# Kernel optimization log

Measured on AMD Instinct MI355X. Metric: run time of the kernel, lower is better.

The kernel has to match this reference:

```python
import jax, jax.numpy as jnp
import numpy as np

B, N, D = 16, 1024, 768
H = 12
HD = D // H
HID = 4 * D
EPS = 1e-6


def _layernorm(x, g, b):
    mu = jnp.mean(x, axis=-1, keepdims=True)
    var = jnp.mean(jnp.square(x - mu), axis=-1, keepdims=True)
    return (x - mu) * jax.lax.rsqrt(var + EPS) * g + b


def setup_inputs() -> dict:
    key = jax.random.key(0)
    ks = jax.random.split(key, 8)
    s_d = 1.0 / np.sqrt(D)
    s_h = 1.0 / np.sqrt(HID)
    return {
        "x": jax.random.normal(ks[0], (B, N, D), dtype=jnp.float32),
        "qkv_w": jax.random.uniform(ks[1], (3 * D, D), jnp.float32, -s_d, s_d),
        "proj_w": jax.random.uniform(ks[2], (D, D), jnp.float32, -s_d, s_d),
        "proj_b": jax.random.uniform(ks[3], (D,), jnp.float32, -s_d, s_d),
        "fc1_w": jax.random.uniform(ks[4], (HID, D), jnp.float32, -s_d, s_d),
        "fc1_b": jax.random.uniform(ks[5], (HID,), jnp.float32, -s_d, s_d),
        "fc2_w": jax.random.uniform(ks[6], (D, HID), jnp.float32, -s_h, s_h),
        "fc2_b": jax.random.uniform(ks[7], (D,), jnp.float32, -s_h, s_h),
        "norm1_g": jnp.ones((D,), jnp.float32),
        "norm1_b": jnp.zeros((D,), jnp.float32),
        "norm2_g": jnp.ones((D,), jnp.float32),
        "norm2_b": jnp.zeros((D,), jnp.float32),
    }


def _attention(x, qkv_w, proj_w, proj_b):
    b, n, _ = x.shape
    qkv = x @ qkv_w.T                                  # [b,n,3D] (no bias: qkv_bias=False)
    qkv = qkv.reshape(b, n, 3, H, HD)
    q, k, v = (jnp.transpose(qkv[:, :, i], (0, 2, 1, 3)) for i in range(3))  # [b,h,n,hd]
    scale = HD ** (-0.5)
    dots = jnp.einsum("bhid,bhjd->bhij", q, k) * scale
    attn = jax.nn.softmax(dots, axis=-1)
    out = jnp.einsum("bhij,bhjd->bhid", attn, v)
    out = jnp.transpose(out, (0, 2, 1, 3)).reshape(b, n, H * HD)
    return out @ proj_w.T + proj_b


def _mlp(x, fc1_w, fc1_b, fc2_w, fc2_b):
    h = jax.nn.gelu(x @ fc1_w.T + fc1_b, approximate=False)
    return h @ fc2_w.T + fc2_b


def reference(x, qkv_w, proj_w, proj_b, fc1_w, fc1_b, fc2_w, fc2_b,
              norm1_g, norm1_b, norm2_g, norm2_b):
    x = x + _attention(_layernorm(x, norm1_g, norm1_b), qkv_w, proj_w, proj_b)
    x = x + _mlp(_layernorm(x, norm2_g, norm2_b), fc1_w, fc1_b, fc2_w, fc2_b)
    return x
```

## Files before the change

### kernel.cpp

```cpp
#include <hip/hip_runtime.h>
#include <hip/hip_bf16.h>
#include <math.h>

using bf16 = __hip_bfloat16;
typedef __attribute__((ext_vector_type(8))) short short8;
typedef __attribute__((ext_vector_type(4))) short shortx4;
typedef __attribute__((ext_vector_type(4))) float floatx4;

#define BB 16
#define NN 1024
#define DD 768
#define HH 12
#define HD 64
#define HID 3072

#define QSCALE 0.1803368801f

__device__ __forceinline__ floatx4 mfma_bf16(short8 a, short8 b, floatx4 c) {
  return __builtin_amdgcn_mfma_f32_16x16x32_bf16(a, b, c, 0, 0, 0);
}

__device__ __forceinline__ short bf16_bits(float f) {
  union { bf16 h; short s; } u;
  u.h = __float2bfloat16(f);
  return u.s;
}

__device__ __forceinline__ void async_copy16(const void* g, void* l) {
  __builtin_amdgcn_global_load_lds(
      (const __attribute__((address_space(1))) unsigned int*)g,
      (__attribute__((address_space(3))) unsigned int*)l,
      16, 0, 0);
}

__device__ __forceinline__ float gelu_f(float x) {
  const float z = x * fmaf(0.10294324f, x * x, 2.3022082f);
  const float e = exp2f(z);
  return x - x * __builtin_amdgcn_rcpf(e + 1.0f);
}

__global__ __launch_bounds__(256)
void cvt_kernel(const float* __restrict__ in, bf16* __restrict__ out, int n4)
{
  const int i = blockIdx.x * 256 + threadIdx.x;
  if (i >= n4) return;
  const float4 v = ((const float4*)in)[i];
  shortx4 o;
  o.x = bf16_bits(v.x); o.y = bf16_bits(v.y);
  o.z = bf16_bits(v.z); o.w = bf16_bits(v.w);
  ((shortx4*)out)[i] = o;
}

__global__ __launch_bounds__(256)
void ln_kernel(const float* __restrict__ x, const float* __restrict__ g,
               const float* __restrict__ b, bf16* __restrict__ y)
{
  const int row = blockIdx.x;
  const int t = threadIdx.x;
  const float* xr = x + (size_t)row * DD;
  float v[3];
  float s = 0.f, s2 = 0.f;
#pragma unroll
  for (int i = 0; i < 3; ++i) {
    float f = xr[t + i * 256];
    v[i] = f;
    s += f;
    s2 += f * f;
  }
#pragma unroll
  for (int off = 1; off < 64; off <<= 1) {
    s  += __shfl_xor(s, off);
    s2 += __shfl_xor(s2, off);
  }
  __shared__ float red[2][4];
  const int wave = t >> 6, lane = t & 63;
  if (lane == 0) { red[0][wave] = s; red[1][wave] = s2; }
  __syncthreads();
  s  = red[0][0] + red[0][1] + red[0][2] + red[0][3];
  s2 = red[1][0] + red[1][1] + red[1][2] + red[1][3];
  const float mu = s * (1.f / DD);
  const float var = s2 * (1.f / DD) - mu * mu;
  const float inv = rsqrtf(var + 1e-6f);
  bf16* yr = y + (size_t)row * DD;
#pragma unroll
  for (int i = 0; i < 3; ++i) {
    int c = t + i * 256;
    yr[c] = __float2bfloat16((v[i] - mu) * inv * g[c] + b[c]);
  }
}

template <int EPI>
__global__ __launch_bounds__(256, 4)
void gemm_kernel(const bf16* __restrict__ A, const bf16* __restrict__ W,
                 const float* __restrict__ bias, const float* __restrict__ res,
                 void* __restrict__ Cv, int N, int K)
{
  __shared__ __align__(16) short smem[16896];
  short* sA = smem;
  short* sB = smem + 8192;

  const int tid  = threadIdx.x;
  const int lane = tid & 63;
  const int wave = tid >> 6;
  const int wm = wave & 1, wn = wave >> 1;
  const int row16 = lane & 15, quad = lane >> 4;

  const int lin = blockIdx.y * gridDim.x + blockIdx.x;
  const int per = gridDim.x * 8;
  const int pan = lin / per, rem = lin % per;
  const int bm = (pan * 8 + (rem & 7)) * 128;
  const int bn = (rem >> 3) * 128;

  const int lrow = lane >> 3;
  const int lkc  = (lane & 7) ^ lrow;

  const bf16* Ag = A + (size_t)(bm + wave * 32 + lrow) * K + lkc * 8;
  const bf16* Bg = W + (size_t)(bn + wave * 32 + lrow) * K + lkc * 8;
  short* sAw = sA + wave * 2048;
  short* sBw = sB + wave * 2048;

  floatx4 acc[4][4] = {};

  for (int kt = 0; kt < K; kt += 64) {
#pragma unroll
    for (int g = 0; g < 4; ++g) {
      async_copy16(Ag + (size_t)g * 8 * K + kt, sAw + g * 512);
      async_copy16(Bg + (size_t)g * 8 * K + kt, sBw + g * 512);
    }
    __syncthreads();
#pragma unroll
    for (int c = 0; c < 2; ++c) {
      short8 af[4], bfr[4];
      const int kc = c * 4 + quad;
#pragma unroll
      for (int mt = 0; mt < 4; ++mt) {
        const int row = wm * 64 + mt * 16 + row16;
        af[mt] = *(const short8*)&sA[(row >> 3) * 512 + ((row & 7) * 8 + (kc ^ (row & 7))) * 8];
      }
#pragma unroll
      for (int nt = 0; nt < 4; ++nt) {
        const int row = wn * 64 + nt * 16 + row16;
        bfr[nt] = *(const short8*)&sB[(row >> 3) * 512 + ((row & 7) * 8 + (kc ^ (row & 7))) * 8];
      }
#pragma unroll
      for (int mt = 0; mt < 4; ++mt)
#pragma unroll
        for (int nt = 0; nt < 4; ++nt)
          acc[mt][nt] = mfma_bf16(bfr[nt], af[mt], acc[mt][nt]);
    }
    __syncthreads();
  }

  if (EPI == 1) {
#pragma unroll
    for (int mt = 0; mt < 4; ++mt) {
      const int row = bm + wm * 64 + mt * 16 + row16;
#pragma unroll
      for (int nt = 0; nt < 4; ++nt) {
        const int col = bn + wn * 64 + nt * 16 + quad * 4;
        const floatx4 bv = *(const floatx4*)&bias[col];
        const floatx4 rv = *(const floatx4*)&res[(size_t)row * N + col];
        floatx4 o;
#pragma unroll
        for (int r = 0; r < 4; ++r) o[r] = acc[mt][nt][r] + bv[r] + rv[r];
        *(floatx4*)&((float*)Cv)[(size_t)row * N + col] = o;
      }
    }
  } else {
    short* sC = smem;
#pragma unroll
    for (int mt = 0; mt < 4; ++mt) {
      const int lr = wm * 64 + mt * 16 + row16;
#pragma unroll
      for (int nt = 0; nt < 4; ++nt) {
        const int lc = wn * 64 + nt * 16 + quad * 4;
        floatx4 bv = {};
        if (EPI == 2) bv = *(const floatx4*)&bias[bn + lc];
        shortx4 pk;
#pragma unroll
        for (int r = 0; r < 4; ++r) {
          float v = acc[mt][nt][r] + bv[r];
          if (EPI == 2) v = gelu_f(v);
          if (EPI == 0 && bn + lc < DD) v *= QSCALE;
          pk[r] = bf16_bits(v);
        }
        *(shortx4*)&sC[lr * 132 + lc] = pk;
      }
    }
    __syncthreads();
#pragma unroll
    for (int it = 0; it < 8; ++it) {
      const int row = (tid >> 4) + it * 16;
      const int col = (tid & 15) * 8;
      short8 v = *(const short8*)&sC[row * 132 + col];
      *(short8*)&((bf16*)Cv)[(size_t)(bm + row) * N + bn + col] = v;
    }
  }
}

__global__ __launch_bounds__(256)
void vtrans_kernel(const bf16* __restrict__ qkv, bf16* __restrict__ vt)
{
  const int bh = blockIdx.y;
  const int b = bh / HH, h = bh % HH;
  const int n0 = blockIdx.x * 64;
  __shared__ __align__(16) short tile[64 * 72];
  const int tid = threadIdx.x;

  const int r = tid >> 2, c16 = (tid & 3) * 16;
  const bf16* src = qkv + (size_t)(b * NN + n0 + r) * 2304 + 2 * DD + h * 64 + c16;
  *(short8*)&tile[r * 72 + c16]     = *(const short8*)(src);
  *(short8*)&tile[r * 72 + c16 + 8] = *(const short8*)(src + 8);
  __syncthreads();

#pragma unroll
  for (int it = 0; it < 2; ++it) {
    const int d  = (tid >> 3) + it * 32;
    const int jg = (tid & 7) * 8;
    short8 o;
#pragma unroll
    for (int t = 0; t < 8; ++t) ((short*)&o)[t] = tile[(jg + t) * 72 + d];
    *(short8*)&vt[((size_t)bh * 64 + d) * NN + n0 + jg] = o;
  }
}

__global__ __launch_bounds__(256, 2)
void attn_kernel(const bf16* __restrict__ qkv, const bf16* __restrict__ vt,
                 bf16* __restrict__ out)
{
  const int nbh = gridDim.y;
  const int gx  = gridDim.x;
  int bh, qi;
  if ((nbh & 7) == 0) {
    const int lin = blockIdx.y * gx + blockIdx.x;
    const int xcd = lin & 7;
    const int idx = lin >> 3;
    const int per = nbh >> 3;
    bh = xcd * per + idx / gx;
    qi = idx % gx;
  } else {
    bh = blockIdx.y; qi = blockIdx.x;
  }
  const int b = bh / HH, h = bh % HH;
  const int q0 = qi * 256;
  const int tid = threadIdx.x;
  const int lane = tid & 63;
  const int wave = tid >> 6;
  const int row16 = lane & 15, quad = lane >> 4;

  __shared__ __align__(16) short sK[4096];
  __shared__ __align__(16) short sVt[4096];
  __shared__ __align__(16) short sP[4][4][1024];

  const bf16* base  = qkv + (size_t)b * NN * 2304 + h * 64;
  const bf16* vbase = vt + (size_t)bh * 64 * NN;

  short8 qf[4][2];
#pragma unroll
  for (int qg = 0; qg < 4; ++qg) {
    const bf16* qrow = base + (size_t)(q0 + wave * 64 + qg * 16 + row16) * 2304;
    qf[qg][0] = *(const short8*)(qrow + quad * 8);
    qf[qg][1] = *(const short8*)(qrow + 32 + quad * 8);
  }

  floatx4 o_acc[4][4] = {};
  floatx4 l_acc[4] = {};
  const short8 ones = { (short)0x3F80, (short)0x3F80, (short)0x3F80, (short)0x3F80,
                        (short)0x3F80, (short)0x3F80, (short)0x3F80, (short)0x3F80 };

  const bf16* ksrc = base + DD + (size_t)(wave * 16 + row16) * 2304 + quad * 8;
  const bf16* vsrc = vbase + (size_t)(wave * 16 + row16) * NN + quad * 8;
  short* kdst = sK + wave * 1024 + lane * 8;
  short* vdst = sVt + wave * 1024 + lane * 8;

  async_copy16(ksrc, kdst);
  async_copy16(ksrc + 32, kdst + 512);
  async_copy16(vsrc, vdst);
  async_copy16(vsrc + 32, vdst + 512);

  for (int jt = 0; jt < NN / 64; ++jt) {
    __syncthreads();

    short8 vb[4][2];
#pragma unroll
    for (int dt = 0; dt < 4; ++dt) {
      vb[dt][0] = *(const short8*)&sVt[dt * 1024 + lane * 8];
      vb[dt][1] = *(const short8*)&sVt[dt * 1024 + 512 + lane * 8];
    }
    short8 kb[4][2];
#pragma unroll
    for (int nt = 0; nt < 4; ++nt) {
      kb[nt][0] = *(const short8*)&sK[nt * 1024 + lane * 8];
      kb[nt][1] = *(const short8*)&sK[nt * 1024 + 512 + lane * 8];
    }
    __syncthreads();

    if (jt + 1 < NN / 64) {
      const bf16* k2 = ksrc + (size_t)(jt + 1) * 64 * 2304;
      const bf16* v2 = vsrc + (jt + 1) * 64;
      async_copy16(k2, kdst);
      async_copy16(k2 + 32, kdst + 512);
      async_copy16(v2, vdst);
      async_copy16(v2 + 32, vdst + 512);
    }

#pragma unroll
    for (int nt = 0; nt < 4; ++nt) {
#pragma unroll
      for (int qg = 0; qg < 4; ++qg) {
        floatx4 st = {};
        st = mfma_bf16(kb[nt][0], qf[qg][0], st);
        st = mfma_bf16(kb[nt][1], qf[qg][1], st);
        const float e0 = exp2f(fminf(st[0], 30.f));
        const float e1 = exp2f(fminf(st[1], 30.f));
        const float e2 = exp2f(fminf(st[2], 30.f));
        const float e3 = exp2f(fminf(st[3], 30.f));
        union { __hip_bfloat162 h2[2]; shortx4 s4; } pu;
        pu.h2[0] = __float22bfloat162_rn(make_float2(e0, e1));
        pu.h2[1] = __float22bfloat162_rn(make_float2(e2, e3));
        *(shortx4*)&sP[wave][qg][(row16 + 16 * (2 * nt + (quad >> 1))) * 8 +
                                 (quad & 1) * 4] = pu.s4;
      }
    }

#pragma unroll
    for (int qg = 0; qg < 4; ++qg) {
      const short8 pf0 = *(const short8*)&sP[wave][qg][lane * 8];
      const short8 pf1 = *(const short8*)&sP[wave][qg][512 + lane * 8];
      l_acc[qg] = mfma_bf16(pf0, ones, l_acc[qg]);
      l_acc[qg] = mfma_bf16(pf1, ones, l_acc[qg]);
#pragma unroll
      for (int dt = 0; dt < 4; ++dt) {
        o_acc[qg][dt] = mfma_bf16(pf0, vb[dt][0], o_acc[qg][dt]);
        o_acc[qg][dt] = mfma_bf16(pf1, vb[dt][1], o_acc[qg][dt]);
      }
    }
  }

#pragma unroll
  for (int qg = 0; qg < 4; ++qg) {
#pragma unroll
    for (int r = 0; r < 4; ++r) {
      const float inv = 1.f / l_acc[qg][r];
      const size_t n = (size_t)(b * NN + q0 + wave * 64 + qg * 16 + quad * 4 + r);
#pragma unroll
      for (int dt = 0; dt < 4; ++dt) {
        out[n * DD + h * 64 + dt * 16 + row16] =
            __float2bfloat16(o_acc[qg][dt][r] * inv);
      }
    }
  }
}

extern "C" void kernel_launch(void* const* d_in, const int* in_sizes, int n_in,
                              void* d_out, int out_size, void* d_ws, size_t ws_size,
                              hipStream_t stream)
{
  const float* x       = (const float*)d_in[0];
  const float* qkv_w   = (const float*)d_in[1];
  const float* proj_w  = (const float*)d_in[2];
  const float* proj_b  = (const float*)d_in[3];
  const float* fc1_w   = (const float*)d_in[4];
  const float* fc1_b   = (const float*)d_in[5];
  const float* fc2_w   = (const float*)d_in[6];
  const float* fc2_b   = (const float*)d_in[7];
  const float* norm1_g = (const float*)d_in[8];
  const float* norm1_b = (const float*)d_in[9];
  const float* norm2_g = (const float*)d_in[10];
  const float* norm2_b = (const float*)d_in[11];
  float* out = (float*)d_out;

  const int M = BB * NN;
  char* ws = (char*)d_ws;

  bf16* wq = (bf16*)ws;
  bf16* wp = wq + (size_t)3 * DD * DD;
  bf16* w1 = wp + (size_t)DD * DD;
  bf16* w2 = w1 + (size_t)HID * DD;
  bf16* xn = w2 + (size_t)DD * HID;
  char* p2 = (char*)(xn + (size_t)M * DD);
  const size_t base_b = (size_t)(p2 - ws);

  int NBc = 1;
  for (int c = 16; c >= 1; c >>= 1)
    if (ws_size >= base_b + (size_t)c * 1024 * 7680) { NBc = c; break; }

  const int Rc = NBc * NN;
  bf16* qkvb = (bf16*)p2;
  bf16* aob  = qkvb + (size_t)Rc * 2304;
  bf16* vtb  = aob  + (size_t)Rc * DD;
  bf16* hb   = (bf16*)p2;

  cvt_kernel<<<(3 * DD * DD / 4 + 255) / 256, 256, 0, stream>>>(qkv_w, wq, 3 * DD * DD / 4);
  cvt_kernel<<<(DD * DD / 4 + 255) / 256, 256, 0, stream>>>(proj_w, wp, DD * DD / 4);
  cvt_kernel<<<(HID * DD / 4 + 255) / 256, 256, 0, stream>>>(fc1_w, w1, HID * DD / 4);
  cvt_kernel<<<(DD * HID / 4 + 255) / 256, 256, 0, stream>>>(fc2_w, w2, DD * HID / 4);

  ln_kernel<<<M, 256, 0, stream>>>(x, norm1_g, norm1_b, xn);

  for (int c = 0; c < BB / NBc; ++c) {
    const size_t r0 = (size_t)c * Rc;
    gemm_kernel<0><<<dim3(3 * DD / 128, Rc / 128), 256, 0, stream>>>(
        xn + r0 * DD, wq, nullptr, nullptr, qkvb, 3 * DD, DD);
    vtrans_kernel<<<dim3(NN / 64, NBc * HH), 256, 0, stream>>>(qkvb, vtb);
    attn_kernel<<<dim3(NN / 256, NBc * HH), 256, 0, stream>>>(qkvb, vtb, aob);
    gemm_kernel<1><<<dim3(DD / 128, Rc / 128), 256, 0, stream>>>(
        aob, wp, proj_b, x + r0 * DD, out + r0 * DD, DD, DD);
  }

  ln_kernel<<<M, 256, 0, stream>>>(out, norm2_g, norm2_b, xn);

  for (int c = 0; c < BB / NBc; ++c) {
    const size_t r0 = (size_t)c * Rc;
    gemm_kernel<2><<<dim3(HID / 128, Rc / 128), 256, 0, stream>>>(
        xn + r0 * DD, w1, fc1_b, nullptr, hb, HID, DD);
    gemm_kernel<1><<<dim3(DD / 128, Rc / 128), 256, 0, stream>>>(
        hb, w2, fc2_b, out + r0 * DD, out + r0 * DD, DD, HID);
  }
}
```

Measured before the change: 555.8 us.

## Add 256x256-tile GEMM kernel with interleaved async prefetch for QKV and FC1

Adds a new 512-thread GEMM kernel with 256x256 output tiles, double-buffered async global-to-LDS copies interleaved with MFMA groups, priority boosts, and a panel-grouped block swizzle. The QKV and FC1 GEMMs now use it instead of the 128x128 kernel. The aim is to raise arithmetic intensity per LDS load and hide memory latency. The costs are 128KB of shared memory per block, which limits occupancy, and a chunked epilogue. The old kernel's bf16 epilogue loses its bias, GELU and scale handling, which is safe only because the EPI 0 and 2 paths no longer call it.

```diff
diff --git a/kernel.cpp b/kernel.cpp
--- a/kernel.cpp
+++ b/kernel.cpp
@@ -174,16 +174,9 @@
 #pragma unroll
       for (int nt = 0; nt < 4; ++nt) {
         const int lc = wn * 64 + nt * 16 + quad * 4;
-        floatx4 bv = {};
-        if (EPI == 2) bv = *(const floatx4*)&bias[bn + lc];
         shortx4 pk;
 #pragma unroll
-        for (int r = 0; r < 4; ++r) {
-          float v = acc[mt][nt][r] + bv[r];
-          if (EPI == 2) v = gelu_f(v);
-          if (EPI == 0 && bn + lc < DD) v *= QSCALE;
-          pk[r] = bf16_bits(v);
-        }
+        for (int r = 0; r < 4; ++r) pk[r] = bf16_bits(acc[mt][nt][r]);
         *(shortx4*)&sC[lr * 132 + lc] = pk;
       }
     }
@@ -195,6 +188,170 @@
       short8 v = *(const short8*)&sC[row * 132 + col];
       *(short8*)&((bf16*)Cv)[(size_t)(bm + row) * N + bn + col] = v;
     }
+  }
+}
+
+template <int EPI>
+__global__ __launch_bounds__(512, 2)
+void gemm256_kernel(const bf16* __restrict__ A, const bf16* __restrict__ W,
+                    const float* __restrict__ bias, bf16* __restrict__ C,
+                    int N, int K)
+{
+  __shared__ __align__(16) short smem[65536];
+
+  const int tid = threadIdx.x, lane = tid & 63, w = tid >> 6;
+  const int wm = w >> 2, wn = w & 3;
+  const int row16 = lane & 15, quad = lane >> 4;
+
+  const int gy = gridDim.y;
+  const int PP = (gy & 7) ? gy : 8;
+  const int lin = blockIdx.y * gridDim.x + blockIdx.x;
+  const int per = gridDim.x * PP;
+  const int pan = lin / per, rem = lin % per;
+  const int bm = (pan * PP + rem % PP) * 256;
+  const int bn = (rem / PP) * 256;
+
+  const int rl = lane & 15, kl = lane >> 4;
+  const bf16* Asrc = A + (size_t)(bm + (w >> 2) * 128 + (w & 3) * 16 + rl) * K + kl * 8;
+  const bf16* Bsrc = W + (size_t)(bn + w * 16 + rl) * K + kl * 8;
+
+  const int NT = K >> 6;
+
+  auto STAGE = [&](int buf, int ab, int h, int kt) {
+    if (ab) {
+      const int band = (w >> 2) * 8 + h * 4 + (w & 3);
+      short* d = smem + buf * 32768 + band * 1024;
+      const bf16* src = Asrc + (size_t)h * 64 * K + kt;
+      async_copy16(src, d);
+      async_copy16(src + 32, d + 512);
+    } else {
+      const int band = h * 8 + w;
+      short* d = smem + buf * 32768 + 16384 + band * 1024;
+      const bf16* src = Bsrc + (size_t)h * 128 * K + kt;
+      async_copy16(src, d);
+      async_copy16(src + 32, d + 512);
+    }
+  };
+
+  floatx4 acc[8][4] = {};
+
+  STAGE(0, 0, 0, 0); STAGE(0, 0, 1, 0); STAGE(0, 1, 0, 0); STAGE(0, 1, 1, 0);
+
+  for (int t = 0; t < NT; ++t) {
+    const int cur = t & 1, nxt = cur ^ 1;
+    const short* sA = smem + cur * 32768;
+    const short* sB = sA + 16384;
+    const int k2 = (t + 1) * 64;
+    const bool pf = (t + 1 < NT);
+
+    asm volatile("s_waitcnt vmcnt(2)" ::: "memory");
+    __builtin_amdgcn_s_barrier();
+    asm volatile("" ::: "memory");
+
+    short8 bfr[4][2];
+#pragma unroll
+    for (int nt = 0; nt < 4; ++nt)
+#pragma unroll
+      for (int kk = 0; kk < 2; ++kk)
+        bfr[nt][kk] = *(const short8*)&sB[((wn * 4 + nt) * 2 + kk) * 512 + lane * 8];
+    short8 af[4][2];
+#pragma unroll
+    for (int mi = 0; mi < 4; ++mi)
+#pragma unroll
+      for (int kk = 0; kk < 2; ++kk)
+        af[mi][kk] = *(const short8*)&sA[((wm * 8 + mi) * 2 + kk) * 512 + lane * 8];
+
+    if (pf) STAGE(nxt, 0, 0, k2);
+    __builtin_amdgcn_s_setprio(1);
+#pragma unroll
+    for (int mi = 0; mi < 4; ++mi)
+#pragma unroll
+      for (int nt = 0; nt < 2; ++nt)
+#pragma unroll
+        for (int kk = 0; kk < 2; ++kk)
+          acc[mi][nt] = mfma_bf16(bfr[nt][kk], af[mi][kk], acc[mi][nt]);
+    __builtin_amdgcn_s_setprio(0);
+
+    if (pf) STAGE(nxt, 0, 1, k2);
+    __builtin_amdgcn_s_setprio(1);
+#pragma unroll
+    for (int mi = 0; mi < 4; ++mi)
+#pragma unroll
+      for (int nt = 2; nt < 4; ++nt)
+#pragma unroll
+        for (int kk = 0; kk < 2; ++kk)
+          acc[mi][nt] = mfma_bf16(bfr[nt][kk], af[mi][kk], acc[mi][nt]);
+    __builtin_amdgcn_s_setprio(0);
+
+    if (pf) asm volatile("s_waitcnt vmcnt(4)" ::: "memory");
+    else    asm volatile("s_waitcnt vmcnt(0)" ::: "memory");
+    __builtin_amdgcn_s_barrier();
+    asm volatile("" ::: "memory");
+
+#pragma unroll
+    for (int mi = 0; mi < 4; ++mi)
+#pragma unroll
+      for (int kk = 0; kk < 2; ++kk)
+        af[mi][kk] = *(const short8*)&sA[((wm * 8 + 4 + mi) * 2 + kk) * 512 + lane * 8];
+
+    if (pf) STAGE(nxt, 1, 0, k2);
+    __builtin_amdgcn_s_setprio(1);
+#pragma unroll
+    for (int mi = 0; mi < 4; ++mi)
+#pragma unroll
+      for (int nt = 0; nt < 2; ++nt)
+#pragma unroll
+        for (int kk = 0; kk < 2; ++kk)
+          acc[4 + mi][nt] = mfma_bf16(bfr[nt][kk], af[mi][kk], acc[4 + mi][nt]);
+    __builtin_amdgcn_s_setprio(0);
+
+    if (pf) STAGE(nxt, 1, 1, k2);
+    __builtin_amdgcn_s_setprio(1);
+#pragma unroll
+    for (int mi = 0; mi < 4; ++mi)
+#pragma unroll
+      for (int nt = 2; nt < 4; ++nt)
+#pragma unroll
+        for (int kk = 0; kk < 2; ++kk)
+          acc[4 + mi][nt] = mfma_bf16(bfr[nt][kk], af[mi][kk], acc[4 + mi][nt]);
+    __builtin_amdgcn_s_setprio(0);
+  }
+
+  __syncthreads();
+  short* sC = smem;
+  for (int p = 0; p < 4; ++p) {
+    if (wm == (p >> 1)) {
+      const int mb = (p & 1) * 4;
+#pragma unroll
+      for (int mi = 0; mi < 4; ++mi) {
+        const int lr = mi * 16 + row16;
+#pragma unroll
+        for (int nt = 0; nt < 4; ++nt) {
+          const int lc = wn * 64 + nt * 16 + quad * 4;
+          floatx4 bv = {};
+          if (EPI == 2) bv = *(const floatx4*)&bias[bn + lc];
+          const bool qs = (EPI == 0) && (bn + lc < DD);
+          shortx4 pk;
+#pragma unroll
+          for (int r = 0; r < 4; ++r) {
+            float v = acc[mb + mi][nt][r];
+            if (EPI == 2) { v += bv[r]; v = gelu_f(v); }
+            if (qs) v *= QSCALE;
+            pk[r] = bf16_bits(v);
+          }
+          *(shortx4*)&sC[lr * 264 + lc] = pk;
+        }
+      }
+    }
+    __syncthreads();
+#pragma unroll
+    for (int it = 0; it < 4; ++it) {
+      const int row = (tid >> 5) + it * 16;
+      const int col = (tid & 31) * 8;
+      short8 v = *(const short8*)&sC[row * 264 + col];
+      *(short8*)&C[(size_t)(bm + p * 64 + row) * N + bn + col] = v;
+    }
+    __syncthreads();
   }
 }
 
@@ -400,8 +557,8 @@
 
   for (int c = 0; c < BB / NBc; ++c) {
     const size_t r0 = (size_t)c * Rc;
-    gemm_kernel<0><<<dim3(3 * DD / 128, Rc / 128), 256, 0, stream>>>(
-        xn + r0 * DD, wq, nullptr, nullptr, qkvb, 3 * DD, DD);
+    gemm256_kernel<0><<<dim3(3 * DD / 256, Rc / 256), 512, 0, stream>>>(
+        xn + r0 * DD, wq, nullptr, qkvb, 3 * DD, DD);
     vtrans_kernel<<<dim3(NN / 64, NBc * HH), 256, 0, stream>>>(qkvb, vtb);
     attn_kernel<<<dim3(NN / 256, NBc * HH), 256, 0, stream>>>(qkvb, vtb, aob);
     gemm_kernel<1><<<dim3(DD / 128, Rc / 128), 256, 0, stream>>>(
@@ -412,8 +569,8 @@
 
   for (int c = 0; c < BB / NBc; ++c) {
     const size_t r0 = (size_t)c * Rc;
-    gemm_kernel<2><<<dim3(HID / 128, Rc / 128), 256, 0, stream>>>(
-        xn + r0 * DD, w1, fc1_b, nullptr, hb, HID, DD);
+    gemm256_kernel<2><<<dim3(HID / 256, Rc / 256), 512, 0, stream>>>(
+        xn + r0 * DD, w1, fc1_b, hb, HID, DD);
     gemm_kernel<1><<<dim3(DD / 128, Rc / 128), 256, 0, stream>>>(
         hb, w2, fc2_b, out + r0 * DD, out + r0 * DD, DD, HID);
   }
```

New measurement: 683.4 us. 1.23x slower.
